# Performance work log

Hardware: AMD Instinct MI355X
Metric: run time of the kernel (lower is better)

## Reference

```python
import jax, jax.numpy as jnp
import numpy as np

N = 65536          # number of atoms (routing tokens)
NUM_SPECIES = 4    # number of per-species expert models
D_IN, D_HID, D_OUT = 256, 1024, 256


def setup_inputs() -> dict:
    key = jax.random.key(0)
    k = jax.random.split(key, 6)
    x = jax.random.normal(k[0], (N, D_IN), dtype=jnp.float32)
    central_species = jax.random.randint(k[1], (N,), 0, NUM_SPECIES, dtype=jnp.int64)
    # Per-species 2-layer MLP experts, stacked along species axis.
    W1 = jax.random.normal(k[2], (NUM_SPECIES, D_IN, D_HID), dtype=jnp.float32) * (1.0 / np.sqrt(D_IN))
    b1 = jnp.zeros((NUM_SPECIES, D_HID), dtype=jnp.float32)
    W2 = jax.random.normal(k[3], (NUM_SPECIES, D_HID, D_OUT), dtype=jnp.float32) * (1.0 / np.sqrt(D_HID))
    b2 = jnp.zeros((NUM_SPECIES, D_OUT), dtype=jnp.float32)
    return {"x": x, "central_species": central_species, "W1": W1, "b1": b1, "W2": W2, "b2": b2}


def reference(x, central_species, W1, b1, W2, b2):
    # Equivalent to: split rows by species (CentralSplitter), apply the
    # species-specific submodel, scatter results back by mask (CentralUniter).
    # Dense-compute-and-select expression: every row receives exactly the
    # output of its own species' expert, identical math to masked gather/scatter.
    num_species = W1.shape[0]
    out = jnp.zeros((x.shape[0], W2.shape[-1]), dtype=x.dtype)
    for s in range(num_species):  # small fixed expert count
        h = jax.nn.silu(x @ W1[s] + b1[s])          # [N, D_HID]
        y = h @ W2[s] + b2[s]                       # [N, D_OUT]
        sel = (central_species == s)[:, None]
        out = out + jnp.where(sel, y, jnp.zeros_like(y))
    return out
```

## Files before the change

kernel.cpp:

```cpp
#include <hip/hip_runtime.h>
#include <hip/hip_bf16.h>


#define N_ATOMS 65536
#define D_IN 256
#define D_HID 1024
#define D_OUT 256
#define TPS 1024

typedef __attribute__((ext_vector_type(8))) short short8;
typedef __attribute__((ext_vector_type(4))) short short4v;
typedef __attribute__((ext_vector_type(4))) float float4e;

#define WS_BUCKET_OFF 256
#define WS_W1_OFF 1048832
#define WS_W2_OFF 3145984

__device__ __forceinline__ short f2bf(float f) {
  unsigned u = __builtin_bit_cast(unsigned, f);
  unsigned r = (u + 0x7FFFu + ((u >> 16) & 1u)) >> 16;
  return (short)r;
}

__global__ void prep_kernel(const float* __restrict__ W1, const float* __restrict__ W2,
                            short* __restrict__ w1sw, short* __restrict__ w2sw,
                            int* __restrict__ cnt) {
  int gid = blockIdx.x * 256 + threadIdx.x;
  if (gid < 64) cnt[gid] = 0;
  int lane = gid & 63;
  int lr = lane & 15;
  int lk = (lane >> 4) * 8;
  if (gid < 131072) {
    int ks = (gid >> 6) & 7;
    int nt = (gid >> 9) & 63;
    int s  = gid >> 15;
    const float* src = W1 + ((size_t)(s * 256 + ks * 32 + lk)) * 1024 + nt * 16 + lr;
    short8 v;
    for (int j = 0; j < 8; ++j) v[j] = f2bf(src[(size_t)j * 1024]);
    *(short8*)(w1sw + (size_t)gid * 8) = v;
  } else {
    int g = gid - 131072;
    int kt = (g >> 6) & 31;
    int nt = (g >> 11) & 15;
    int s  = g >> 15;
    const float* src = W2 + ((size_t)(s * 1024 + kt * 32 + lk)) * 256 + nt * 16 + lr;
    short8 v;
    for (int j = 0; j < 8; ++j) v[j] = f2bf(src[(size_t)j * 256]);
    *(short8*)(w2sw + (size_t)g * 8) = v;
  }
}

#define CF_BLOCKS 32
#define CF_ITERS 8
__global__ void count_fill_kernel(const int* __restrict__ species,
                                  int* __restrict__ cnt, int* __restrict__ bucket) {
  int tid = threadIdx.x;
  int lane = tid & 63, wid = tid >> 6;
  __shared__ int wcnt[CF_ITERS][4][4];
  __shared__ int wb[CF_ITERS][4][4];
  __shared__ int base_sm[4];
  int sv[CF_ITERS], rk[CF_ITERS];
  unsigned long long below = (1ull << lane) - 1ull;
  int base_i = blockIdx.x * (CF_ITERS * 256);
  #pragma unroll
  for (int it = 0; it < CF_ITERS; ++it) {
    int s = species[base_i + it * 256 + tid] & 3;
    sv[it] = s;
    unsigned long long m0 = __ballot(s == 0);
    unsigned long long m1 = __ballot(s == 1);
    unsigned long long m2 = __ballot(s == 2);
    unsigned long long m3 = __ballot(s == 3);
    unsigned long long ms = (s == 0) ? m0 : (s == 1) ? m1 : (s == 2) ? m2 : m3;
    rk[it] = __popcll(ms & below);
    if (lane == 0) {
      wcnt[it][wid][0] = __popcll(m0);
      wcnt[it][wid][1] = __popcll(m1);
      wcnt[it][wid][2] = __popcll(m2);
      wcnt[it][wid][3] = __popcll(m3);
    }
  }
  __syncthreads();
  if (tid < 4) {
    int ss = tid, run = 0;
    for (int it = 0; it < CF_ITERS; ++it)
      for (int w = 0; w < 4; ++w) {
        wb[it][w][ss] = run;
        run += wcnt[it][w][ss];
      }
    base_sm[ss] = atomicAdd(&cnt[ss * 16], run);
  }
  __syncthreads();
  #pragma unroll
  for (int it = 0; it < CF_ITERS; ++it) {
    int ss = sv[it];
    bucket[ss * N_ATOMS + base_sm[ss] + wb[it][wid][ss] + rk[it]] = base_i + it * 256 + tid;
  }
}

#define XS_STRIDE 280
#define HS_STRIDE 152
__global__ __launch_bounds__(256, 2) void fused_kernel(
    const float* __restrict__ x, const int* __restrict__ cntArr,
    const int* __restrict__ bucket, const short* __restrict__ w1sw,
    const short* __restrict__ w2sw, const float* __restrict__ b1,
    const float* __restrict__ b2, float* __restrict__ out) {
  int bid = blockIdx.x;
  int s = (bid & 7) >> 1;
  int t = ((bid >> 3) << 1) | (bid & 1);
  int cnt = cntArr[s * 16];
  int r0 = t * 64;
  if (r0 >= cnt) return;
  int nrows = min(64, cnt - r0);
  const int* buck = bucket + s * N_ATOMS + r0;

  __shared__ short Xs[64 * XS_STRIDE];
  __shared__ short Hs[2][64 * HS_STRIDE];

  int tid = threadIdx.x;

  for (int i = 0; i < 8; ++i) {
    int id = tid + i * 256;
    int r = id >> 5;
    int g = id & 31;
    short8 v = {};
    if (r < nrows) {
      const float4* src = (const float4*)(x + (size_t)buck[r] * D_IN + g * 8);
      float4 f0 = src[0];
      float4 f1 = src[1];
      v[0] = f2bf(f0.x); v[1] = f2bf(f0.y); v[2] = f2bf(f0.z); v[3] = f2bf(f0.w);
      v[4] = f2bf(f1.x); v[5] = f2bf(f1.y); v[6] = f2bf(f1.z); v[7] = f2bf(f1.w);
    }
    *(short8*)(Xs + r * XS_STRIDE + g * 8) = v;
  }

  int lane = tid & 63;
  int wid = tid >> 6;
  int lr = lane & 15;
  int lk = (lane >> 4) * 8;
  int lq = (lane >> 4) * 4;

  int rowIdx[4];
  #pragma unroll
  for (int bt = 0; bt < 4; ++bt) {
    int r = bt * 16 + lr;
    rowIdx[bt] = (r < nrows) ? buck[r] : -1;
  }

  float4e accY[4][4];
  #pragma unroll
  for (int at = 0; at < 4; ++at) {
    float4e bv = *(const float4e*)(b2 + s * D_OUT + wid * 64 + at * 16 + lq);
    #pragma unroll
    for (int bt = 0; bt < 4; ++bt) accY[at][bt] = bv;
  }

  short8 b1f[16];
  #pragma unroll
  for (int ks = 0; ks < 8; ++ks)
    #pragma unroll
    for (int at = 0; at < 2; ++at) {
      int nt = 0 * 8 + wid * 2 + at;
      b1f[ks * 2 + at] = *(const short8*)(w1sw + ((size_t)((s * 64 + nt) * 8 + ks)) * 512 + lane * 8);
    }

  __syncthreads();

  for (int c = 0; c < 8; ++c) {
    float4e acc1[2][4];
    #pragma unroll
    for (int at = 0; at < 2; ++at) {
      float4e bv = *(const float4e*)(b1 + s * D_HID + c * 128 + wid * 32 + at * 16 + lq);
      #pragma unroll
      for (int bt = 0; bt < 4; ++bt) acc1[at][bt] = bv;
    }
    #pragma unroll
    for (int ks = 0; ks < 8; ++ks) {
      short8 xb[4];
      #pragma unroll
      for (int bt = 0; bt < 4; ++bt)
        xb[bt] = *(const short8*)(Xs + (bt * 16 + lr) * XS_STRIDE + ks * 32 + lk);
      #pragma unroll
      for (int at = 0; at < 2; ++at)
        #pragma unroll
        for (int bt = 0; bt < 4; ++bt)
          acc1[at][bt] = __builtin_amdgcn_mfma_f32_16x16x32_bf16(b1f[ks * 2 + at], xb[bt], acc1[at][bt], 0, 0, 0);
    }
    short8 b2f[16];
    #pragma unroll
    for (int ks = 0; ks < 4; ++ks)
      #pragma unroll
      for (int at = 0; at < 4; ++at) {
        int nt = wid * 4 + at;
        int kt = c * 4 + ks;
        b2f[ks * 4 + at] = *(const short8*)(w2sw + ((size_t)((s * 16 + nt) * 32 + kt)) * 512 + lane * 8);
      }
    short* hsb = Hs[c & 1];
    #pragma unroll
    for (int at = 0; at < 2; ++at) {
      int hidloc = wid * 32 + at * 16 + lq;
      #pragma unroll
      for (int bt = 0; bt < 4; ++bt) {
        float4e v4 = acc1[at][bt];
        short4v hv;
        #pragma unroll
        for (int q = 0; q < 4; ++q) {
          float pre = v4[q];
          float val = pre * __builtin_amdgcn_rcpf(1.0f + __expf(-pre));
          hv[q] = f2bf(val);
        }
        *(short4v*)(hsb + (bt * 16 + lr) * HS_STRIDE + hidloc) = hv;
      }
    }
    __syncthreads();
    if (c < 7) {
      #pragma unroll
      for (int ks = 0; ks < 8; ++ks)
        #pragma unroll
        for (int at = 0; at < 2; ++at) {
          int nt = (c + 1) * 8 + wid * 2 + at;
          b1f[ks * 2 + at] = *(const short8*)(w1sw + ((size_t)((s * 64 + nt) * 8 + ks)) * 512 + lane * 8);
        }
    }
    #pragma unroll
    for (int ks = 0; ks < 4; ++ks) {
      short8 hb[4];
      #pragma unroll
      for (int bt = 0; bt < 4; ++bt)
        hb[bt] = *(const short8*)(hsb + (bt * 16 + lr) * HS_STRIDE + ks * 32 + lk);
      #pragma unroll
      for (int at = 0; at < 4; ++at)
        #pragma unroll
        for (int bt = 0; bt < 4; ++bt)
          accY[at][bt] = __builtin_amdgcn_mfma_f32_16x16x32_bf16(b2f[ks * 4 + at], hb[bt], accY[at][bt], 0, 0, 0);
    }
  }

  #pragma unroll
  for (int at = 0; at < 4; ++at) {
    int nb = wid * 64 + at * 16 + lq;
    #pragma unroll
    for (int bt = 0; bt < 4; ++bt) {
      if (rowIdx[bt] >= 0)
        *(float4e*)(out + (size_t)rowIdx[bt] * D_OUT + nb) = accY[at][bt];
    }
  }
}

extern "C" void kernel_launch(void* const* d_in, const int* in_sizes, int n_in,
                              void* d_out, int out_size, void* d_ws, size_t ws_size,
                              hipStream_t stream) {
  const float* x  = (const float*)d_in[0];
  const int* spc  = (const int*)d_in[1];
  const float* W1 = (const float*)d_in[2];
  const float* b1 = (const float*)d_in[3];
  const float* W2 = (const float*)d_in[4];
  const float* b2 = (const float*)d_in[5];
  float* out = (float*)d_out;

  int*   cnt    = (int*)d_ws;
  int*   bucket = (int*)((char*)d_ws + WS_BUCKET_OFF);
  short* w1sw   = (short*)((char*)d_ws + WS_W1_OFF);
  short* w2sw   = (short*)((char*)d_ws + WS_W2_OFF);

  prep_kernel<<<1024, 256, 0, stream>>>(W1, W2, w1sw, w2sw, cnt);
  count_fill_kernel<<<CF_BLOCKS, 256, 0, stream>>>(spc, cnt, bucket);
  fused_kernel<<<4 * TPS, 256, 0, stream>>>(x, cnt, bucket, w1sw, w2sw, b1, b2, out);
}
```

Baseline: 226.2 us.

## Use 512-thread blocks with 8 waves splitting hidden and output tiles

```diff
diff --git a/kernel.cpp b/kernel.cpp
--- a/kernel.cpp
+++ b/kernel.cpp
@@ -97,9 +97,9 @@
   }
 }
 
-#define XS_STRIDE 280
-#define HS_STRIDE 152
-__global__ __launch_bounds__(256, 2) void fused_kernel(
+#define XS_STRIDE 264
+#define HS_STRIDE 140
+__global__ __launch_bounds__(512, 4) void fused_kernel(
     const float* __restrict__ x, const int* __restrict__ cntArr,
     const int* __restrict__ bucket, const short* __restrict__ w1sw,
     const short* __restrict__ w2sw, const float* __restrict__ b1,
@@ -118,8 +118,8 @@
 
   int tid = threadIdx.x;
 
-  for (int i = 0; i < 8; ++i) {
-    int id = tid + i * 256;
+  for (int i = 0; i < 4; ++i) {
+    int id = tid + i * 512;
     int r = id >> 5;
     int g = id & 31;
     short8 v = {};
@@ -146,32 +146,28 @@
     rowIdx[bt] = (r < nrows) ? buck[r] : -1;
   }
 
-  float4e accY[4][4];
-  #pragma unroll
-  for (int at = 0; at < 4; ++at) {
-    float4e bv = *(const float4e*)(b2 + s * D_OUT + wid * 64 + at * 16 + lq);
+  float4e accY[2][4];
+  #pragma unroll
+  for (int at = 0; at < 2; ++at) {
+    float4e bv = *(const float4e*)(b2 + s * D_OUT + wid * 32 + at * 16 + lq);
     #pragma unroll
     for (int bt = 0; bt < 4; ++bt) accY[at][bt] = bv;
   }
 
-  short8 b1f[16];
-  #pragma unroll
-  for (int ks = 0; ks < 8; ++ks)
-    #pragma unroll
-    for (int at = 0; at < 2; ++at) {
-      int nt = 0 * 8 + wid * 2 + at;
-      b1f[ks * 2 + at] = *(const short8*)(w1sw + ((size_t)((s * 64 + nt) * 8 + ks)) * 512 + lane * 8);
-    }
-
   __syncthreads();
 
   for (int c = 0; c < 8; ++c) {
-    float4e acc1[2][4];
-    #pragma unroll
-    for (int at = 0; at < 2; ++at) {
-      float4e bv = *(const float4e*)(b1 + s * D_HID + c * 128 + wid * 32 + at * 16 + lq);
-      #pragma unroll
-      for (int bt = 0; bt < 4; ++bt) acc1[at][bt] = bv;
+    short8 b1f[8];
+    #pragma unroll
+    for (int ks = 0; ks < 8; ++ks) {
+      int nt = c * 8 + wid;
+      b1f[ks] = *(const short8*)(w1sw + ((size_t)((s * 64 + nt) * 8 + ks)) * 512 + lane * 8);
+    }
+    float4e acc1[4];
+    {
+      float4e bv = *(const float4e*)(b1 + s * D_HID + c * 128 + wid * 16 + lq);
+      #pragma unroll
+      for (int bt = 0; bt < 4; ++bt) acc1[bt] = bv;
     }
     #pragma unroll
     for (int ks = 0; ks < 8; ++ks) {
@@ -180,47 +176,35 @@
       for (int bt = 0; bt < 4; ++bt)
         xb[bt] = *(const short8*)(Xs + (bt * 16 + lr) * XS_STRIDE + ks * 32 + lk);
       #pragma unroll
-      for (int at = 0; at < 2; ++at)
-        #pragma unroll
-        for (int bt = 0; bt < 4; ++bt)
-          acc1[at][bt] = __builtin_amdgcn_mfma_f32_16x16x32_bf16(b1f[ks * 2 + at], xb[bt], acc1[at][bt], 0, 0, 0);
-    }
-    short8 b2f[16];
+      for (int bt = 0; bt < 4; ++bt)
+        acc1[bt] = __builtin_amdgcn_mfma_f32_16x16x32_bf16(b1f[ks], xb[bt], acc1[bt], 0, 0, 0);
+    }
+    short8 b2f[8];
     #pragma unroll
     for (int ks = 0; ks < 4; ++ks)
       #pragma unroll
-      for (int at = 0; at < 4; ++at) {
-        int nt = wid * 4 + at;
+      for (int at = 0; at < 2; ++at) {
+        int nt = wid * 2 + at;
         int kt = c * 4 + ks;
-        b2f[ks * 4 + at] = *(const short8*)(w2sw + ((size_t)((s * 16 + nt) * 32 + kt)) * 512 + lane * 8);
+        b2f[ks * 2 + at] = *(const short8*)(w2sw + ((size_t)((s * 16 + nt) * 32 + kt)) * 512 + lane * 8);
       }
     short* hsb = Hs[c & 1];
-    #pragma unroll
-    for (int at = 0; at < 2; ++at) {
-      int hidloc = wid * 32 + at * 16 + lq;
+    {
+      int hidloc = wid * 16 + lq;
       #pragma unroll
       for (int bt = 0; bt < 4; ++bt) {
-        float4e v4 = acc1[at][bt];
-        short4v hv;
+        float4e v4 = acc1[bt];
+        short4v h;
         #pragma unroll
         for (int q = 0; q < 4; ++q) {
           float pre = v4[q];
           float val = pre * __builtin_amdgcn_rcpf(1.0f + __expf(-pre));
-          hv[q] = f2bf(val);
+          h[q] = f2bf(val);
         }
-        *(short4v*)(hsb + (bt * 16 + lr) * HS_STRIDE + hidloc) = hv;
+        *(short4v*)(hsb + (bt * 16 + lr) * HS_STRIDE + hidloc) = h;
       }
     }
     __syncthreads();
-    if (c < 7) {
-      #pragma unroll
-      for (int ks = 0; ks < 8; ++ks)
-        #pragma unroll
-        for (int at = 0; at < 2; ++at) {
-          int nt = (c + 1) * 8 + wid * 2 + at;
-          b1f[ks * 2 + at] = *(const short8*)(w1sw + ((size_t)((s * 64 + nt) * 8 + ks)) * 512 + lane * 8);
-        }
-    }
     #pragma unroll
     for (int ks = 0; ks < 4; ++ks) {
       short8 hb[4];
@@ -228,16 +212,16 @@
       for (int bt = 0; bt < 4; ++bt)
         hb[bt] = *(const short8*)(hsb + (bt * 16 + lr) * HS_STRIDE + ks * 32 + lk);
       #pragma unroll
-      for (int at = 0; at < 4; ++at)
+      for (int at = 0; at < 2; ++at)
         #pragma unroll
         for (int bt = 0; bt < 4; ++bt)
-          accY[at][bt] = __builtin_amdgcn_mfma_f32_16x16x32_bf16(b2f[ks * 4 + at], hb[bt], accY[at][bt], 0, 0, 0);
-    }
-  }
-
-  #pragma unroll
-  for (int at = 0; at < 4; ++at) {
-    int nb = wid * 64 + at * 16 + lq;
+          accY[at][bt] = __builtin_amdgcn_mfma_f32_16x16x32_bf16(b2f[ks * 2 + at], hb[bt], accY[at][bt], 0, 0, 0);
+    }
+  }
+
+  #pragma unroll
+  for (int at = 0; at < 2; ++at) {
+    int nb = wid * 32 + at * 16 + lq;
     #pragma unroll
     for (int bt = 0; bt < 4; ++bt) {
       if (rowIdx[bt] >= 0)
@@ -264,5 +248,5 @@
 
   prep_kernel<<<1024, 256, 0, stream>>>(W1, W2, w1sw, w2sw, cnt);
   count_fill_kernel<<<CF_BLOCKS, 256, 0, stream>>>(spc, cnt, bucket);
-  fused_kernel<<<4 * TPS, 256, 0, stream>>>(x, cnt, bucket, w1sw, w2sw, b1, b2, out);
-}
+  fused_kernel<<<4 * TPS, 512, 0, stream>>>(x, cnt, bucket, w1sw, w2sw, b1, b2, out);
+}
```

Measured after the change: 315.9 us. 39.7% more time.
